# Optimization experiments

Hardware: AMD Instinct MI355X
Metric: run time of the kernel (lower is better)

Reference implementation:

```python
import jax, jax.numpy as jnp
import numpy as np

N_NODES = 100_000
N_EDGES = 1_000_000
D_X = 8
H = 128
N_DOM = 32768
N_BND = 8192
RE = 1.0 / 1.45e-05  # Reynolds number used in momentum residuals


def setup_inputs() -> dict:
    key = jax.random.key(0)
    ks = jax.random.split(key, 16)
    s = 0.05
    return {
        "x": jax.random.normal(ks[0], (N_NODES, D_X), jnp.float32),
        "x_mask": jax.random.uniform(ks[1], (N_NODES, 6), dtype=jnp.float32),
        "edge_index": jax.random.randint(ks[2], (2, N_EDGES), 0, N_NODES),
        "edge_attr": jax.random.normal(ks[3], (N_EDGES, 4), jnp.float32),
        "pos": jax.random.normal(ks[4], (N_NODES, 3), jnp.float32),
        "batch": jnp.zeros((N_NODES,), jnp.int32),
        "domain_sampling_points": jax.random.normal(ks[5], (N_DOM, 2), jnp.float32),
        "boundary_sampling_points": jax.random.normal(ks[6], (N_BND, 2), jnp.float32),
        "idxs_boundary_sampled": jax.random.randint(ks[7], (N_BND,), 0, N_NODES),
        # surrogate net parameters
        "Wx": jax.random.normal(ks[8], (D_X, H), jnp.float32) * s,
        "Wp": jax.random.normal(ks[9], (2, H), jnp.float32) * s,
        "We": jax.random.normal(ks[10], (3, H), jnp.float32) * s,
        "Wout": jax.random.normal(ks[11], (H, 3), jnp.float32) * s,
        "W1": jax.random.normal(ks[12], (2 + H, H), jnp.float32) * s,
        "b1": jnp.zeros((H,), jnp.float32),
        "W2": jax.random.normal(ks[13], (H, H), jnp.float32) * s,
        "b2": jnp.zeros((H,), jnp.float32),
        "W3": jax.random.normal(ks[14], (H, 3), jnp.float32) * s,
    }


def reference(x, x_mask, edge_index, edge_attr, pos, batch,
              domain_sampling_points, boundary_sampling_points,
              idxs_boundary_sampled,
              Wx, Wp, We, Wout, W1, b1, W2, b2, W3):
    pos2 = pos[:, :2]                              # pos = pos[:, :2]
    ea = edge_attr[:, jnp.array([0, 1, 3])]        # edge_attr[:, [0,1,3]]

    # --- surrogate GNN: one message-passing layer -> supervised output ---
    node_h = jnp.tanh(x @ Wx + pos2 @ Wp)          # [N, H]
    src, dst = edge_index[0], edge_index[1]
    msg = node_h[src] * (ea @ We)                  # [E, H] large gather (memory-bound)
    agg = jax.ops.segment_sum(msg, dst, num_segments=node_h.shape[0])
    h = jnp.tanh(node_h + agg)                     # [N, H]
    out_sup = h @ Wout                             # [N, 3]
    ctx = h.mean(axis=0)                           # [H] pooled graph context (constant wrt sp)

    # --- per-point coordinate network (u, v, p) ---
    def f_samp(sp):
        z = jnp.concatenate([sp, ctx])
        h1 = jnp.tanh(z @ W1 + b1)
        h2 = jnp.tanh(h1 @ W2 + b2)
        return h2 @ W3                             # [3] -> (u, v, p)

    sp = jnp.concatenate([domain_sampling_points, boundary_sampling_points])  # [S, 2]
    out_samp = jax.vmap(f_samp)(sp)                            # [S, 3]
    grads = jax.vmap(jax.jacrev(f_samp))(sp)                   # [S, 3, 2]
    hess = jax.vmap(jax.jacrev(jax.jacrev(f_samp)))(sp)        # [S, 3, 2, 2]

    nd = domain_sampling_points.shape[0]
    # --- domain (full_laminar) residuals ---
    u, v = out_samp[:nd, 0], out_samp[:nd, 1]
    u_x, u_y = grads[:nd, 0, 0], grads[:nd, 0, 1]
    v_x, v_y = grads[:nd, 1, 0], grads[:nd, 1, 1]
    p_x, p_y = grads[:nd, 2, 0], grads[:nd, 2, 1]
    u_xx, u_yy = hess[:nd, 0, 0, 0], hess[:nd, 0, 1, 1]
    v_xx, v_yy = hess[:nd, 1, 0, 0], hess[:nd, 1, 1, 1]
    continuity = u_x + v_y
    momentum_x = u * u_x + v * u_y + p_x - (u_xx + u_yy) / RE
    momentum_y = u * v_x + v * v_y + p_y - (v_xx + v_yy) / RE

    # --- boundary-condition residuals (vmapped BC math) ---
    bu, bv, bp = out_samp[nd:, 0], out_samp[nd:, 1], out_samp[nd:, 2]
    bu_x, bv_y = grads[nd:, 0, 0], grads[nd:, 1, 1]
    bp_x, bp_y = grads[nd:, 2, 0], grads[nd:, 2, 1]
    x_BC = x[idxs_boundary_sampled]                # [B, D_X]
    m = x_mask[idxs_boundary_sampled]              # [B, 6]
    t_x, t_y = x_BC[:, 0], x_BC[:, 1]
    n_x, n_y = -t_y, t_x
    r_vt = jnp.abs(t_x * bu + t_y * bv - x_BC[:, 2]) * m[:, 1]
    r_vn = jnp.abs(n_x * bu + n_y * bv - x_BC[:, 3]) * m[:, 2]
    r_p = jnp.abs(bp - x_BC[:, 4]) * m[:, 3]
    r_dvdn = jnp.abs(n_x * bu_x + n_y * bv_y - x_BC[:, 5]) * m[:, 4]
    r_dpdn = jnp.abs(n_x * bp_x + n_y * bp_y - x_BC[:, 6]) * m[:, 5]
    c = m[:, 1:6].sum(axis=1)
    boundary = (r_vt + r_vn + r_p + r_dvdn + r_dpdn) / c

    return (out_sup, continuity, momentum_x, momentum_y, boundary)
```

## Files before the change

kernel.cpp:

```cpp
#include <hip/hip_runtime.h>
#include <hip/hip_fp8.h>
#include <math.h>

#define H 128
#define DXI 8
#define NNODES 100000
#define NEDGES 1000000
#define NRUNS (NEDGES / 64)
#define NDOM 32768
#define NBND 8192
#define NPTS (NDOM + NBND)
#define INV_RE 1.45e-05f
#define NODE_BLOCKS 1024
#define NPR (NNODES / 8)

#define NSB ((NNODES + 1023) / 1024)

#define CONT_OFF (NNODES * 3)
#define MOMX_OFF (CONT_OFF + NDOM)
#define MOMY_OFF (MOMX_OFF + NDOM)
#define BND_OFF  (MOMY_OFF + NDOM)

#define KPAD 136
#define A_STRIDE (32 * KPAD)

typedef __attribute__((ext_vector_type(8))) short short8;
typedef __attribute__((ext_vector_type(4))) float f32x4;

__device__ __forceinline__ float fast_tanh(float x) {
    const float e = __builtin_amdgcn_exp2f(x * 2.88539008f);
    return fmaf(-2.f, __builtin_amdgcn_rcpf(e + 1.f), 1.f);
}

__device__ __forceinline__ unsigned pack_bf16(float a, float b) {
    unsigned ua = __float_as_uint(a), ub = __float_as_uint(b);
    ua += 0x7fffu + ((ua >> 16) & 1u);
    ub += 0x7fffu + ((ub >> 16) & 1u);
    return (ua >> 16) | (ub & 0xffff0000u);
}

__device__ __forceinline__ short to_bf16(float f) {
    unsigned u = __float_as_uint(f);
    u += 0x7fffu + ((u >> 16) & 1u);
    return (short)(u >> 16);
}

__global__ __launch_bounds__(256) void hist_kernel(
    const int* __restrict__ eidx, int* __restrict__ counts)
{
    const int* dst = eidx + NEDGES;
    for (int e = blockIdx.x * 256 + threadIdx.x; e < NEDGES; e += gridDim.x * 256)
        atomicAdd(&counts[dst[e]], 1);
}

__global__ __launch_bounds__(256) void scan1_kernel(
    const int* __restrict__ counts, int* __restrict__ excl, int* __restrict__ bsum,
    const float* __restrict__ x, const float* __restrict__ pos,
    const float* __restrict__ Wx, const float* __restrict__ Wp,
    unsigned short* __restrict__ th, uint4* __restrict__ agg4)
{
    const int tid = threadIdx.x;

    if (blockIdx.x < NSB) {
        const int b = blockIdx.x;
        const int base = b * 1024 + tid * 4;
        int v0 = 0, v1 = 0, v2 = 0, v3 = 0;
        if (base + 3 < NNODES) {
            const int4 t = *(const int4*)(counts + base);
            v0 = t.x; v1 = t.y; v2 = t.z; v3 = t.w;
        } else {
            if (base     < NNODES) v0 = counts[base];
            if (base + 1 < NNODES) v1 = counts[base + 1];
            if (base + 2 < NNODES) v2 = counts[base + 2];
            if (base + 3 < NNODES) v3 = counts[base + 3];
        }
        const int own = v0 + v1 + v2 + v3;
        int s = own;
        const int lane = tid & 63, wv = tid >> 6;
#pragma unroll
        for (int d = 1; d < 64; d <<= 1) {
            const int t = __shfl_up(s, d);
            if (lane >= d) s += t;
        }
        __shared__ int wsum[4];
        if (lane == 63) wsum[wv] = s;
        __syncthreads();
        int woff = 0;
        for (int w = 0; w < wv; ++w) woff += wsum[w];
        const int e0 = s - own + woff;
        const int e1 = e0 + v0, e2 = e1 + v1, e3 = e2 + v2;
        if (base + 3 < NNODES) {
            *(int4*)(excl + base) = make_int4(e0, e1, e2, e3);
        } else {
            if (base     < NNODES) excl[base]     = e0;
            if (base + 1 < NNODES) excl[base + 1] = e1;
            if (base + 2 < NNODES) excl[base + 2] = e2;
            if (base + 3 < NNODES) excl[base + 3] = e3;
        }
        if (tid == 0) bsum[b] = wsum[0] + wsum[1] + wsum[2] + wsum[3];
    }

    const int gid = blockIdx.x * 256 + tid;
    const uint4 z = make_uint4(0u, 0u, 0u, 0u);
    for (size_t i = gid; i < (size_t)NNODES * 16; i += (size_t)gridDim.x * 256)
        agg4[i] = z;

    const int lane = tid & 63;
    const int wv   = tid >> 6;
    const int c0 = lane * 2, c1 = c0 + 1;
    float wxa[DXI], wxb_[DXI];
#pragma unroll
    for (int k = 0; k < DXI; ++k) { wxa[k] = Wx[k * H + c0]; wxb_[k] = Wx[k * H + c1]; }
    const float wp00 = Wp[c0], wp01 = Wp[H + c0];
    const float wp10 = Wp[c1], wp11 = Wp[H + c1];

    for (int n = blockIdx.x * 4 + wv; n < NNODES; n += gridDim.x * 4) {
        const float* xr = x + (size_t)n * DXI;
        const float px = pos[(size_t)n * 3], py = pos[(size_t)n * 3 + 1];
        float a0 = fmaf(wp00, px, wp01 * py);
        float a1 = fmaf(wp10, px, wp11 * py);
#pragma unroll
        for (int k = 0; k < DXI; ++k) {
            const float xv = xr[k];
            a0 = fmaf(xv, wxa[k], a0);
            a1 = fmaf(xv, wxb_[k], a1);
        }
        const __hip_fp8_e4m3 q0(fast_tanh(a0));
        const __hip_fp8_e4m3 q1(fast_tanh(a1));
        th[(size_t)n * 64 + lane] =
            (unsigned short)((unsigned)q0.__x | ((unsigned)q1.__x << 8));
    }
}

__global__ __launch_bounds__(128) void scan2_kernel(int* __restrict__ bsum)
{
    const int tid = threadIdx.x;
    int v = (tid < NSB) ? bsum[tid] : 0;
    const int own = v;
    const int lane = tid & 63, wv = tid >> 6;
#pragma unroll
    for (int d = 1; d < 64; d <<= 1) {
        const int t = __shfl_up(v, d);
        if (lane >= d) v += t;
    }
    __shared__ int ws2[2];
    if (lane == 63) ws2[wv] = v;
    __syncthreads();
    if (wv == 1) v += ws2[0];
    if (tid < NSB) bsum[tid] = v - own;
}

__global__ __launch_bounds__(256) void scan3_kernel(
    int* __restrict__ offsets, int* __restrict__ cursor, const int* __restrict__ bsum)
{
    const int tid = threadIdx.x, b = blockIdx.x;
    const int base = b * 1024 + tid * 4;
    const int add = bsum[b];
    if (base + 3 < NNODES) {
        int4 t = *(const int4*)(offsets + base);
        t.x += add; t.y += add; t.z += add; t.w += add;
        *(int4*)(offsets + base) = t;
        *(int4*)(cursor + base) = t;
    } else {
        for (int i = 0; i < 4; ++i)
            if (base + i < NNODES) {
                const int t = offsets[base + i] + add;
                offsets[base + i] = t;
                cursor[base + i] = t;
            }
    }
}

__global__ __launch_bounds__(256) void scatter_kernel(
    const int* __restrict__ eidx, const float* __restrict__ eattr,
    int* __restrict__ cursor, uint4* __restrict__ csrE)
{
    const int* dst = eidx + NEDGES;
    const int G   = gridDim.x >> 3;
    const int g   = blockIdx.x >> 3;
    const int r   = blockIdx.x & 7;
    const int dlo = r * NPR, dhi = dlo + NPR;
    for (int e = g * 256 + threadIdx.x; e < NEDGES; e += G * 256) {
        const int d = dst[e];
        if (d >= dlo && d < dhi) {
            const float4 ea = ((const float4*)eattr)[e];
            const int slot = atomicAdd(&cursor[d], 1);
            uint4 rec;
            rec.x = (unsigned)eidx[e];
            rec.y = (unsigned)d;
            rec.z = pack_bf16(ea.x, ea.y);
            rec.w = pack_bf16(ea.w, 0.f);
            csrE[slot] = rec;
        }
    }
}

__global__ __launch_bounds__(256) void seg_edge_kernel(
    const uint4* __restrict__ csrE, const unsigned short* __restrict__ th,
    const float* __restrict__ We, unsigned* __restrict__ agg)
{
    const int run = blockIdx.x * 4 + (threadIdx.x >> 6);
    if (run >= NRUNS) return;
    const int lane = threadIdx.x & 63;
    const int c0 = lane * 2, c1 = c0 + 1;

    const float wea0 = We[c0], wea1 = We[H + c0], wea2 = We[2 * H + c0];
    const float web0 = We[c1], web1 = We[H + c1], web2 = We[2 * H + c1];

    const uint4 rec = csrE[(size_t)run * 64 + lane];
    const int mydst = (int)rec.y;

    float acc0 = 0.f, acc1 = 0.f;
    bool first = true;
    int cur = __builtin_amdgcn_readlane(mydst, 0);

#pragma unroll
    for (int sub = 0; sub < 4; ++sub) {
        unsigned short rowv[16];
#pragma unroll
        for (int t = 0; t < 16; ++t) {
            const int s = __builtin_amdgcn_readlane((int)rec.x, sub * 16 + t);
            rowv[t] = th[(size_t)s * 64 + lane];
        }
#pragma unroll
        for (int t = 0; t < 16; ++t) {
            const int e = sub * 16 + t;
            const unsigned ue01 = (unsigned)__builtin_amdgcn_readlane((int)rec.z, e);
            const unsigned ue3  = (unsigned)__builtin_amdgcn_readlane((int)rec.w, e);
            const float e0f = __uint_as_float(ue01 << 16);
            const float e1f = __uint_as_float(ue01 & 0xffff0000u);
            const float e3f = __uint_as_float(ue3 << 16);
            __hip_fp8_e4m3 d0, d1;
            d0.__x = (__hip_fp8_storage_t)(rowv[t] & 0xff);
            d1.__x = (__hip_fp8_storage_t)(rowv[t] >> 8);
            const float th0 = (float)d0;
            const float th1 = (float)d1;
            const float w0 = fmaf(e0f, wea0, fmaf(e1f, wea1, e3f * wea2));
            const float w1 = fmaf(e0f, web0, fmaf(e1f, web1, e3f * web2));
            acc0 = fmaf(th0, w0, acc0);
            acc1 = fmaf(th1, w1, acc1);

            const int nxt = (e < 63) ? __builtin_amdgcn_readlane(mydst, e + 1) : -1;
            if (nxt != cur) {
                unsigned* p = agg + (size_t)cur * 64 + lane;
                if (first || e == 63) {
                    unsigned old = *p;
                    while (true) {
                        const float g0 = __uint_as_float(old << 16) + acc0;
                        const float g1 = __uint_as_float(old & 0xffff0000u) + acc1;
                        const unsigned nw = pack_bf16(g0, g1);
                        const unsigned prev = atomicCAS(p, old, nw);
                        if (prev == old) break;
                        old = prev;
                    }
                } else {
                    *p = pack_bf16(acc0, acc1);
                }
                acc0 = 0.f; acc1 = 0.f;
                first = false;
                cur = nxt;
            }
        }
    }
}

__global__ __launch_bounds__(256) void node_kernel(
    const float* __restrict__ x, const float* __restrict__ pos,
    const unsigned* __restrict__ agg,
    const float* __restrict__ Wx, const float* __restrict__ Wp,
    const float* __restrict__ Wout,
    float* __restrict__ out_sup, float* __restrict__ ctx_part)
{
    const int lane = threadIdx.x & 63;
    const int wv   = threadIdx.x >> 6;
    const int c0 = lane * 2, c1 = c0 + 1;

    float wxa[DXI], wxb_[DXI];
#pragma unroll
    for (int k = 0; k < DXI; ++k) { wxa[k] = Wx[k * H + c0]; wxb_[k] = Wx[k * H + c1]; }
    const float wp00 = Wp[c0], wp01 = Wp[H + c0];
    const float wp10 = Wp[c1], wp11 = Wp[H + c1];
    const float woa0 = Wout[c0 * 3], woa1 = Wout[c0 * 3 + 1], woa2 = Wout[c0 * 3 + 2];
    const float wob0 = Wout[c1 * 3], wob1 = Wout[c1 * 3 + 1], wob2 = Wout[c1 * 3 + 2];

    float ctx0 = 0.f, ctx1 = 0.f;

    for (int n = blockIdx.x * 4 + wv; n < NNODES; n += gridDim.x * 4) {
        const unsigned ag = agg[(size_t)n * 64 + lane];
        const float* xr = x + (size_t)n * DXI;
        const float px = pos[(size_t)n * 3], py = pos[(size_t)n * 3 + 1];
        float a0 = fmaf(wp00, px, wp01 * py);
        float a1 = fmaf(wp10, px, wp11 * py);
#pragma unroll
        for (int k = 0; k < DXI; ++k) {
            const float xv = xr[k];
            a0 = fmaf(xv, wxa[k], a0);
            a1 = fmaf(xv, wxb_[k], a1);
        }
        const float h0 = fast_tanh(fast_tanh(a0) + __uint_as_float(ag << 16));
        const float h1 = fast_tanh(fast_tanh(a1) + __uint_as_float(ag & 0xffff0000u));
        ctx0 += h0; ctx1 += h1;

        float p0 = fmaf(h0, woa0, h1 * wob0);
        float p1 = fmaf(h0, woa1, h1 * wob1);
        float p2 = fmaf(h0, woa2, h1 * wob2);
#pragma unroll
        for (int m = 32; m; m >>= 1) {
            p0 += __shfl_xor(p0, m);
            p1 += __shfl_xor(p1, m);
            p2 += __shfl_xor(p2, m);
        }
        if (lane == 0) {
            out_sup[(size_t)n * 3 + 0] = p0;
            out_sup[(size_t)n * 3 + 1] = p1;
            out_sup[(size_t)n * 3 + 2] = p2;
        }
    }

    __shared__ float part[4][H];
    part[wv][c0] = ctx0;
    part[wv][c1] = ctx1;
    __syncthreads();
    if (threadIdx.x < H) {
        const int ch = threadIdx.x;
        ctx_part[(size_t)blockIdx.x * H + ch] =
            part[0][ch] + part[1][ch] + part[2][ch] + part[3][ch];
    }
}

__global__ __launch_bounds__(128) void ctx_kernel(
    const float* __restrict__ ctx_part, const float* __restrict__ W1,
    const float* __restrict__ b1, float* __restrict__ tab)
{
    __shared__ float ctx[H];
    const int ch = threadIdx.x;
    float s0 = 0.f, s1 = 0.f, s2 = 0.f, s3 = 0.f;
#pragma unroll 4
    for (int b = 0; b < NODE_BLOCKS; b += 4) {
        s0 += ctx_part[(size_t)(b + 0) * H + ch];
        s1 += ctx_part[(size_t)(b + 1) * H + ch];
        s2 += ctx_part[(size_t)(b + 2) * H + ch];
        s3 += ctx_part[(size_t)(b + 3) * H + ch];
    }
    ctx[ch] = (s0 + s1 + s2 + s3) * (1.0f / (float)NNODES);
    __syncthreads();
    float acc = b1[ch];
    for (int k = 0; k < H; ++k) acc = fmaf(ctx[k], W1[(size_t)(2 + k) * H + ch], acc);
    const float A0 = W1[ch], A1 = W1[H + ch];
    tab[ch * 8 + 0] = A0;
    tab[ch * 8 + 1] = A1;
    tab[ch * 8 + 2] = acc;
    tab[ch * 8 + 3] = A0 * A0;
    tab[ch * 8 + 4] = A1 * A1;
    tab[ch * 8 + 5] = 0.f;
    tab[ch * 8 + 6] = 0.f;
    tab[ch * 8 + 7] = 0.f;
}

__global__ __launch_bounds__(256, 2) void samp_mfma_kernel(
    const float* __restrict__ dom, const float* __restrict__ bnd,
    const int* __restrict__ bidx,
    const float* __restrict__ x, const float* __restrict__ xmask,
    const float* __restrict__ tab,
    const float* __restrict__ W2, const float* __restrict__ b2,
    const float* __restrict__ W3, float* __restrict__ out)
{
    __shared__ __attribute__((aligned(16))) short Bt[128 * KPAD];
    __shared__ __attribute__((aligned(16))) short Alds[5 * A_STRIDE];
    __shared__ __attribute__((aligned(16))) float red[32][13];

    const int tid = threadIdx.x;
    const int blk = blockIdx.x;

    for (int i = tid; i < H * H; i += 256) {
        const int k = i >> 7, n = i & 127;
        Bt[n * KPAD + k] = to_bf16(W2[i]);
    }

    for (int idx = tid; idx < 32 * 64; idx += 256) {
        const int pl = idx >> 6;
        const int k0 = (idx & 63) * 2;
        const int p  = blk * 32 + pl;
        float spx, spy;
        if (p < NDOM) { spx = dom[(size_t)p * 2];          spy = dom[(size_t)p * 2 + 1]; }
        else          { spx = bnd[(size_t)(p - NDOM) * 2]; spy = bnd[(size_t)(p - NDOM) * 2 + 1]; }
        float v[2][5];
#pragma unroll
        for (int kk = 0; kk < 2; ++kk) {
            const int k = k0 + kk;
            const float4 t4 = *(const float4*)(tab + (size_t)k * 8);
            const float A1s = tab[(size_t)k * 8 + 4];
            const float A0 = t4.x, A1 = t4.y, cc = t4.z, A0s = t4.w;
            const float a1 = fmaf(spx, A0, fmaf(spy, A1, cc));
            const float e  = __builtin_amdgcn_exp2f(a1 * 2.88539008f);
            const float h1 = fmaf(-2.f, __builtin_amdgcn_rcpf(e + 1.f), 1.f);
            const float t1 = fmaf(-h1, h1, 1.f);
            const float m2 = -2.f * h1 * t1;
            v[kk][0] = h1;
            v[kk][1] = t1 * A0;
            v[kk][2] = t1 * A1;
            v[kk][3] = m2 * A0s;
            v[kk][4] = m2 * A1s;
        }
        const int base = pl * KPAD + k0;
#pragma unroll
        for (int q = 0; q < 5; ++q)
            *(unsigned*)&Alds[q * A_STRIDE + base] = pack_bf16(v[0][q], v[1][q]);
    }
    __syncthreads();

    const int lane = tid & 63;
    const int wv = tid >> 6;
    const int pt = wv >> 1;
    const int jh = wv & 1;
    const int ln = lane & 15;
    const int hi = lane >> 4;

    f32x4 acc[4][5];
#pragma unroll
    for (int nt = 0; nt < 4; ++nt)
#pragma unroll
        for (int q = 0; q < 5; ++q)
            acc[nt][q] = (f32x4){0.f, 0.f, 0.f, 0.f};

#pragma unroll
    for (int kc = 0; kc < 4; ++kc) {
        short8 af[5];
#pragma unroll
        for (int q = 0; q < 5; ++q)
            af[q] = *(const short8*)&Alds[q * A_STRIDE + (pt * 16 + ln) * KPAD + kc * 32 + hi * 8];
        short8 bfr[4];
#pragma unroll
        for (int nt = 0; nt < 4; ++nt)
            bfr[nt] = *(const short8*)&Bt[(jh * 64 + nt * 16 + ln) * KPAD + kc * 32 + hi * 8];
#pragma unroll
        for (int nt = 0; nt < 4; ++nt)
#pragma unroll
            for (int q = 0; q < 5; ++q)
                acc[nt][q] = __builtin_amdgcn_mfma_f32_16x16x32_bf16(af[q], bfr[nt], acc[nt][q], 0, 0, 0);
    }

    float w30[4], w31[4], w32[4], b2j[4];
#pragma unroll
    for (int nt = 0; nt < 4; ++nt) {
        const int j = jh * 64 + nt * 16 + ln;
        w30[nt] = W3[j * 3];
        w31[nt] = W3[j * 3 + 1];
        w32[nt] = W3[j * 3 + 2];
        b2j[nt] = b2[j];
    }

    float rr[4][13];
#pragma unroll
    for (int i = 0; i < 4; ++i)
#pragma unroll
        for (int c = 0; c < 13; ++c) rr[i][c] = 0.f;

#pragma unroll
    for (int i = 0; i < 4; ++i) {
#pragma unroll
        for (int nt = 0; nt < 4; ++nt) {
            const float a2v  = acc[nt][0][i] + b2j[nt];
            const float d2xv = acc[nt][1][i];
            const float d2yv = acc[nt][2][i];
            const float exxv = acc[nt][3][i];
            const float eyyv = acc[nt][4][i];
            const float h2 = fast_tanh(a2v);
            const float t2 = fmaf(-h2, h2, 1.f);
            const float gx = t2 * d2xv;
            const float gy = t2 * d2yv;
            const float hxx = fmaf(-2.f * h2 * gx, d2xv, t2 * exxv);
            const float hyy = fmaf(-2.f * h2 * gy, d2yv, t2 * eyyv);
            rr[i][0]  = fmaf(h2, w30[nt], rr[i][0]);
            rr[i][1]  = fmaf(h2, w31[nt], rr[i][1]);
            rr[i][2]  = fmaf(h2, w32[nt], rr[i][2]);
            rr[i][3]  = fmaf(gx, w30[nt], rr[i][3]);
            rr[i][4]  = fmaf(gx, w31[nt], rr[i][4]);
            rr[i][5]  = fmaf(gx, w32[nt], rr[i][5]);
            rr[i][6]  = fmaf(gy, w30[nt], rr[i][6]);
            rr[i][7]  = fmaf(gy, w31[nt], rr[i][7]);
            rr[i][8]  = fmaf(gy, w32[nt], rr[i][8]);
            rr[i][9]  = fmaf(hxx, w30[nt], rr[i][9]);
            rr[i][10] = fmaf(hxx, w31[nt], rr[i][10]);
            rr[i][11] = fmaf(hyy, w30[nt], rr[i][11]);
            rr[i][12] = fmaf(hyy, w31[nt], rr[i][12]);
        }
    }

#pragma unroll
    for (int m = 1; m < 16; m <<= 1)
#pragma unroll
        for (int i = 0; i < 4; ++i)
#pragma unroll
            for (int c = 0; c < 13; ++c)
                rr[i][c] += __shfl_xor(rr[i][c], m);

    if (ln == 0 && jh == 0) {
#pragma unroll
        for (int i = 0; i < 4; ++i) {
            const int pl = pt * 16 + hi * 4 + i;
#pragma unroll
            for (int c = 0; c < 13; ++c) red[pl][c] = rr[i][c];
        }
    }
    __syncthreads();
    if (ln == 0 && jh == 1) {
#pragma unroll
        for (int i = 0; i < 4; ++i) {
            const int pl = pt * 16 + hi * 4 + i;
#pragma unroll
            for (int c = 0; c < 13; ++c) red[pl][c] += rr[i][c];
        }
    }
    __syncthreads();

    if (tid < 32) {
        const int p = blk * 32 + tid;
        float s[13];
#pragma unroll
        for (int c = 0; c < 13; ++c) s[c] = red[tid][c];
        const float u = s[0], v = s[1], pp = s[2];
        const float ux = s[3], vx = s[4], px = s[5];
        const float uy = s[6], vy = s[7], py = s[8];
        const float uxx = s[9], vxx = s[10], uyy = s[11], vyy = s[12];
        if (p < NDOM) {
            out[CONT_OFF + p] = ux + vy;
            out[MOMX_OFF + p] = fmaf(u, ux, fmaf(v, uy, px)) - (uxx + uyy) * INV_RE;
            out[MOMY_OFF + p] = fmaf(u, vx, fmaf(v, vy, py)) - (vxx + vyy) * INV_RE;
        } else {
            const int i = p - NDOM;
            const int idx = bidx[i];
            const float* xbp = x + (size_t)idx * DXI;
            const float* mm = xmask + (size_t)idx * 6;
            const float tx = xbp[0], ty = xbp[1];
            const float nx = -ty, ny = tx;
            const float r_vt = fabsf(tx * u + ty * v - xbp[2]) * mm[1];
            const float r_vn = fabsf(nx * u + ny * v - xbp[3]) * mm[2];
            const float r_p  = fabsf(pp - xbp[4]) * mm[3];
            const float r_dv = fabsf(nx * ux + ny * vy - xbp[5]) * mm[4];
            const float r_dp = fabsf(nx * px + ny * py - xbp[6]) * mm[5];
            const float c = mm[1] + mm[2] + mm[3] + mm[4] + mm[5];
            out[BND_OFF + i] = (r_vt + r_vn + r_p + r_dv + r_dp) / c;
        }
    }
}

extern "C" void kernel_launch(void* const* d_in, const int* in_sizes, int n_in,
                              void* d_out, int out_size, void* d_ws, size_t ws_size,
                              hipStream_t stream) {
    const float* x     = (const float*)d_in[0];
    const float* xmask = (const float*)d_in[1];
    const int*   eidx  = (const int*)d_in[2];
    const float* eattr = (const float*)d_in[3];
    const float* pos   = (const float*)d_in[4];
    const float* dom   = (const float*)d_in[6];
    const float* bnd   = (const float*)d_in[7];
    const int*   bidx  = (const int*)d_in[8];
    const float* Wx    = (const float*)d_in[9];
    const float* Wp    = (const float*)d_in[10];
    const float* We    = (const float*)d_in[11];
    const float* Wout  = (const float*)d_in[12];
    const float* W1    = (const float*)d_in[13];
    const float* b1    = (const float*)d_in[14];
    const float* W2    = (const float*)d_in[15];
    const float* b2    = (const float*)d_in[16];
    const float* W3    = (const float*)d_in[17];

    float* out = (float*)d_out;

    int*            counts   = (int*)d_ws;
    int*            offsets  = counts + NNODES;
    int*            cursor   = offsets + NNODES + 8;
    int*            bsum     = cursor + NNODES;
    uint4*          csrE     = (uint4*)(bsum + 128);
    unsigned short* th       = (unsigned short*)(csrE + NEDGES);
    unsigned*       agg      = (unsigned*)(th + (size_t)NNODES * 64);
    float*          ctx_part = (float*)(agg + (size_t)NNODES * 64);
    float*          tab      = ctx_part + (size_t)NODE_BLOCKS * H;

    (void)hipMemsetAsync(counts, 0, (size_t)NNODES * sizeof(int), stream);

    hist_kernel<<<1024, 256, 0, stream>>>(eidx, counts);
    scan1_kernel<<<2048, 256, 0, stream>>>(counts, offsets, bsum, x, pos, Wx, Wp, th, (uint4*)agg);
    scan2_kernel<<<1, 128, 0, stream>>>(bsum);
    scan3_kernel<<<NSB, 256, 0, stream>>>(offsets, cursor, bsum);
    scatter_kernel<<<4096, 256, 0, stream>>>(eidx, eattr, cursor, csrE);
    seg_edge_kernel<<<(NRUNS + 3) / 4, 256, 0, stream>>>(csrE, th, We, agg);
    node_kernel<<<NODE_BLOCKS, 256, 0, stream>>>(x, pos, agg, Wx, Wp, Wout, out, ctx_part);
    ctx_kernel<<<1, H, 0, stream>>>(ctx_part, W1, b1, tab);
    samp_mfma_kernel<<<NPTS / 32, 256, 0, stream>>>(dom, bnd, bidx, x, xmask, tab, W2, b2, W3, out);
}
```

Baseline: 255.9 us.

## Pack CSR edge records into 8 bytes with fp8 attributes and chunked scatter

Edge records shrink from 16 bytes (src, dst, bf16 attrs) to 8 bytes: 17-bit src, 17-bit dst and three fp8 e4m3 edge attributes packed into a 64-bit word. This halves record write traffic in the scatter and read traffic in the segmented edge kernel. The scatter kernel also switches from a grid-stride loop to contiguous edge chunks per block group, and its block-index mapping is reordered so blocks covering the same chunk across destination ranges are spaced apart. Edge attributes lose precision by going to fp8, and 17-bit indices rely on the node count staying below 131072.

```diff
diff --git a/kernel.cpp b/kernel.cpp
--- a/kernel.cpp
+++ b/kernel.cpp
@@ -14,6 +14,9 @@
 #define NODE_BLOCKS 1024
 #define NPR (NNODES / 8)
 
+#define NCHUNK 512
+#define CHUNKE ((NEDGES + NCHUNK - 1) / NCHUNK)
+
 #define NSB ((NNODES + 1023) / 1024)
 
 #define CONT_OFF (NNODES * 3)
@@ -43,6 +46,12 @@
     unsigned u = __float_as_uint(f);
     u += 0x7fffu + ((u >> 16) & 1u);
     return (short)(u >> 16);
+}
+
+__device__ __forceinline__ float fp8_dec(unsigned b) {
+    __hip_fp8_e4m3 d;
+    d.__x = (__hip_fp8_storage_t)b;
+    return (float)d;
 }
 
 __global__ __launch_bounds__(256) void hist_kernel(
@@ -173,30 +182,37 @@
 
 __global__ __launch_bounds__(256) void scatter_kernel(
     const int* __restrict__ eidx, const float* __restrict__ eattr,
-    int* __restrict__ cursor, uint4* __restrict__ csrE)
+    int* __restrict__ cursor, uint2* __restrict__ csrE)
 {
     const int* dst = eidx + NEDGES;
-    const int G   = gridDim.x >> 3;
-    const int g   = blockIdx.x >> 3;
-    const int r   = blockIdx.x & 7;
+    const int bid = blockIdx.x;
+    const int q = bid & 7;
+    const int t = bid >> 3;
+    const int k = t >> 3;
+    const int r = t & 7;
+    const int g = q * (NCHUNK / 8) + k;
     const int dlo = r * NPR, dhi = dlo + NPR;
-    for (int e = g * 256 + threadIdx.x; e < NEDGES; e += G * 256) {
+    const int ebeg = g * CHUNKE;
+    const int eend = min(ebeg + CHUNKE, NEDGES);
+    for (int e = ebeg + threadIdx.x; e < eend; e += 256) {
         const int d = dst[e];
         if (d >= dlo && d < dhi) {
             const float4 ea = ((const float4*)eattr)[e];
             const int slot = atomicAdd(&cursor[d], 1);
-            uint4 rec;
-            rec.x = (unsigned)eidx[e];
-            rec.y = (unsigned)d;
-            rec.z = pack_bf16(ea.x, ea.y);
-            rec.w = pack_bf16(ea.w, 0.f);
-            csrE[slot] = rec;
+            const __hip_fp8_e4m3 f0(ea.x), f1(ea.y), f3(ea.w);
+            const unsigned long long v =
+                (unsigned long long)(unsigned)eidx[e]
+              | ((unsigned long long)(unsigned)d << 17)
+              | ((unsigned long long)f0.__x << 34)
+              | ((unsigned long long)f1.__x << 42)
+              | ((unsigned long long)f3.__x << 50);
+            csrE[slot] = make_uint2((unsigned)v, (unsigned)(v >> 32));
         }
     }
 }
 
 __global__ __launch_bounds__(256) void seg_edge_kernel(
-    const uint4* __restrict__ csrE, const unsigned short* __restrict__ th,
+    const uint2* __restrict__ csrE, const unsigned short* __restrict__ th,
     const float* __restrict__ We, unsigned* __restrict__ agg)
 {
     const int run = blockIdx.x * 4 + (threadIdx.x >> 6);
@@ -207,8 +223,9 @@
     const float wea0 = We[c0], wea1 = We[H + c0], wea2 = We[2 * H + c0];
     const float web0 = We[c1], web1 = We[H + c1], web2 = We[2 * H + c1];
 
-    const uint4 rec = csrE[(size_t)run * 64 + lane];
-    const int mydst = (int)rec.y;
+    const uint2 rec = csrE[(size_t)run * 64 + lane];
+    const int mysrc = (int)(rec.x & 0x1FFFFu);
+    const int mydst = (int)((rec.x >> 17) | ((rec.y & 3u) << 15));
 
     float acc0 = 0.f, acc1 = 0.f;
     bool first = true;
@@ -219,22 +236,18 @@
         unsigned short rowv[16];
 #pragma unroll
         for (int t = 0; t < 16; ++t) {
-            const int s = __builtin_amdgcn_readlane((int)rec.x, sub * 16 + t);
+            const int s = __builtin_amdgcn_readlane(mysrc, sub * 16 + t);
             rowv[t] = th[(size_t)s * 64 + lane];
         }
 #pragma unroll
         for (int t = 0; t < 16; ++t) {
             const int e = sub * 16 + t;
-            const unsigned ue01 = (unsigned)__builtin_amdgcn_readlane((int)rec.z, e);
-            const unsigned ue3  = (unsigned)__builtin_amdgcn_readlane((int)rec.w, e);
-            const float e0f = __uint_as_float(ue01 << 16);
-            const float e1f = __uint_as_float(ue01 & 0xffff0000u);
-            const float e3f = __uint_as_float(ue3 << 16);
-            __hip_fp8_e4m3 d0, d1;
-            d0.__x = (__hip_fp8_storage_t)(rowv[t] & 0xff);
-            d1.__x = (__hip_fp8_storage_t)(rowv[t] >> 8);
-            const float th0 = (float)d0;
-            const float th1 = (float)d1;
+            const unsigned hi = (unsigned)__builtin_amdgcn_readlane((int)rec.y, e);
+            const float e0f = fp8_dec((hi >> 2) & 0xffu);
+            const float e1f = fp8_dec((hi >> 10) & 0xffu);
+            const float e3f = fp8_dec((hi >> 18) & 0xffu);
+            const float th0 = fp8_dec(rowv[t] & 0xffu);
+            const float th1 = fp8_dec((unsigned)rowv[t] >> 8);
             const float w0 = fmaf(e0f, wea0, fmaf(e1f, wea1, e3f * wea2));
             const float w1 = fmaf(e0f, web0, fmaf(e1f, web1, e3f * web2));
             acc0 = fmaf(th0, w0, acc0);
@@ -572,7 +585,7 @@
     int*            offsets  = counts + NNODES;
     int*            cursor   = offsets + NNODES + 8;
     int*            bsum     = cursor + NNODES;
-    uint4*          csrE     = (uint4*)(bsum + 128);
+    uint2*          csrE     = (uint2*)(bsum + 128);
     unsigned short* th       = (unsigned short*)(csrE + NEDGES);
     unsigned*       agg      = (unsigned*)(th + (size_t)NNODES * 64);
     float*          ctx_part = (float*)(agg + (size_t)NNODES * 64);
@@ -584,7 +597,7 @@
     scan1_kernel<<<2048, 256, 0, stream>>>(counts, offsets, bsum, x, pos, Wx, Wp, th, (uint4*)agg);
     scan2_kernel<<<1, 128, 0, stream>>>(bsum);
     scan3_kernel<<<NSB, 256, 0, stream>>>(offsets, cursor, bsum);
-    scatter_kernel<<<4096, 256, 0, stream>>>(eidx, eattr, cursor, csrE);
+    scatter_kernel<<<NCHUNK * 8, 256, 0, stream>>>(eidx, eattr, cursor, csrE);
     seg_edge_kernel<<<(NRUNS + 3) / 4, 256, 0, stream>>>(csrE, th, We, agg);
     node_kernel<<<NODE_BLOCKS, 256, 0, stream>>>(x, pos, agg, Wx, Wp, Wout, out, ctx_part);
     ctx_kernel<<<1, H, 0, stream>>>(ctx_part, W1, b1, tab);
```

After: 255.8 us. No clear change (-0.0%).
